# Kernel optimization log

Measured on AMD Instinct MI355X. Metric: run time of the kernel, lower is better.

The kernel has to match this reference:

```python
import jax, jax.numpy as jnp
import numpy as np

DMODEL = 1024
NHEAD = 16
DHEAD = DMODEL // NHEAD

def _layernorm(x, g, b, eps=1e-5):
    mu = jnp.mean(x, axis=-1, keepdims=True)
    var = jnp.var(x, axis=-1, keepdims=True)
    return (x - mu) * jax.lax.rsqrt(var + eps) * g + b

def setup_inputs() -> dict:
    key = jax.random.key(0)
    ks = jax.random.split(key, 12)
    b, lq, lv, d = 2, 2048, 2048, DMODEL
    s = 1.0 / np.sqrt(d)
    return {
        "q": jax.random.normal(ks[0], (b, lq, d), jnp.float32),
        "k": jax.random.normal(ks[1], (b, lv, d), jnp.float32),
        "v": jax.random.normal(ks[2], (b, lv, d), jnp.float32),
        "qln_g": jnp.ones((d,), jnp.float32),
        "qln_b": jnp.zeros((d,), jnp.float32),
        "kvln_g": jnp.ones((d,), jnp.float32),
        "kvln_b": jnp.zeros((d,), jnp.float32),
        "Wq": jax.random.normal(ks[3], (d, d), jnp.float32) * s,
        "Wk": jax.random.normal(ks[4], (d, d), jnp.float32) * s,
        "Wv": jax.random.normal(ks[5], (d, d), jnp.float32) * s,
        "Wg": jax.random.normal(ks[6], (d, d), jnp.float32) * s,
        "bg": jnp.zeros((d,), jnp.float32),
        "Wo": jax.random.normal(ks[7], (d, d), jnp.float32) * s,
    }

def reference(q, k, v, qln_g, qln_b, kvln_g, kvln_b, Wq, Wk, Wv, Wg, bg, Wo):
    b, lq, d = q.shape
    lv = v.shape[1]
    qn = _layernorm(q, qln_g, qln_b)           # [b, lq, d]
    q_ = qn @ Wq.T
    kk = _layernorm(k, kvln_g, kvln_b) @ Wk.T
    vv = _layernorm(v, kvln_g, kvln_b) @ Wv.T
    qh = q_.reshape(b, lq, NHEAD, DHEAD)       # bqhd
    kh = kk.reshape(b, lv, NHEAD, DHEAD)
    vh = vv.reshape(b, lv, NHEAD, DHEAD)
    scores = jnp.einsum('bqhd,bkhd->bhqk', qh, kh) / np.sqrt(DHEAD)
    attn = jax.nn.softmax(scores, axis=-1)
    y = jnp.einsum('bhqk,bkhd->bqhd', attn, vh).reshape(b, lq, d)
    g = jax.nn.sigmoid(qn @ Wg.T + bg)
    return (y * g) @ Wo.T
```

## Files before the change

kernel.cpp:

```cpp
#include <hip/hip_runtime.h>
#include <hip/hip_bf16.h>

#define DMODEL 1024
#define NHEAD  16
#define DHEAD  64
#define BATCH  2
#define LQ     2048
#define LV     2048
#define ROWS   (BATCH*LQ)
#define WELEMS (DMODEL*DMODEL)
#define BH     (BATCH*NHEAD)

typedef short bf16x8 __attribute__((ext_vector_type(8)));
typedef float f32x4  __attribute__((ext_vector_type(4)));

__device__ __forceinline__ float bf2f(unsigned short s) {
    union { unsigned u; float f; } v; v.u = ((unsigned)s) << 16;
    return v.f;
}
__device__ __forceinline__ unsigned pk_bf(float a, float b) {
    union { __hip_bfloat162 h; unsigned u; } c;
    c.h = __float22bfloat162_rn(make_float2(a, b));
    return c.u;
}

__device__ __forceinline__ void cp16_g2l(const void* g, void* l) {
    __builtin_amdgcn_global_load_lds(
        (const __attribute__((address_space(1))) void*)g,
        (__attribute__((address_space(3))) void*)l,
        16, 0, 0);
}

#define QSCALE (0.125f * 1.4426950408889634f)

__global__ __launch_bounds__(256) void prep_kernel(
    const float* q, const float* k, const float* v,
    const float* qg, const float* qb, const float* kvg, const float* kvb,
    const float* Wq, const float* Wk, const float* Wv, const float* Wg, const float* Wo,
    unsigned short* qn, unsigned short* kn, unsigned short* vn, unsigned short* wb)
{
    __shared__ float rs[4], rq[4];
    int z = blockIdx.y;
    if (z < 5) {
        if (blockIdx.x >= WELEMS / 1024) return;
        const float* srcs[5] = {Wq, Wk, Wv, Wg, Wo};
        const float* s = srcs[z];
        unsigned short* d = wb + (size_t)z * WELEMS;
        int i = (blockIdx.x * 256 + threadIdx.x) * 4;
        float4 x = *(const float4*)(s + i);
        uint2 o = make_uint2(pk_bf(x.x, x.y), pk_bf(x.z, x.w));
        *(uint2*)(d + i) = o;
        return;
    }
    int row = blockIdx.x;
    const float *x, *gp, *bp; unsigned short* o;
    if      (z == 5) { x = q; gp = qg;  bp = qb;  o = qn; }
    else if (z == 6) { x = k; gp = kvg; bp = kvb; o = kn; }
    else             { x = v; gp = kvg; bp = kvb; o = vn; }

    int col = threadIdx.x * 4;
    float4 xv = *(const float4*)(x + (size_t)row * DMODEL + col);
    float s  = xv.x + xv.y + xv.z + xv.w;
    float sq = xv.x*xv.x + xv.y*xv.y + xv.z*xv.z + xv.w*xv.w;
    #pragma unroll
    for (int off = 1; off < 64; off <<= 1) { s += __shfl_xor(s, off); sq += __shfl_xor(sq, off); }

    int wave = threadIdx.x >> 6, lane = threadIdx.x & 63;
    if (lane == 0) { rs[wave] = s; rq[wave] = sq; }
    __syncthreads();
    float ts = rs[0] + rs[1] + rs[2] + rs[3];
    float tq = rq[0] + rq[1] + rq[2] + rq[3];
    float mu  = ts * (1.0f / DMODEL);
    float var = tq * (1.0f / DMODEL) - mu * mu;
    float inv = rsqrtf(var + 1e-5f);

    float4 gv = *(const float4*)(gp + col);
    float4 bv = *(const float4*)(bp + col);
    float r0 = (xv.x - mu) * inv * gv.x + bv.x;
    float r1 = (xv.y - mu) * inv * gv.y + bv.y;
    float r2 = (xv.z - mu) * inv * gv.z + bv.z;
    float r3 = (xv.w - mu) * inv * gv.w + bv.w;
    *(uint2*)(o + (size_t)row * DMODEL + col) = make_uint2(pk_bf(r0, r1), pk_bf(r2, r3));
}

template<int MODE>
__device__ __forceinline__ void gemm256_core(
    const unsigned short* A, const unsigned short* Bw,
    unsigned short* Obf, const float* bias, float scale,
    unsigned short* Al, unsigned short* Bl, int bm, int bn)
{
    int tid  = threadIdx.x;
    int w = tid >> 6, l = tid & 63, quad = l >> 4, L = l & 15;
    int wm = w >> 2, wn = w & 3;

    int srow = w * 16 + (l >> 2);
    int scol = (l & 3) * 8;
    const unsigned short* gA = A  + (size_t)(bm * 256 + srow) * DMODEL + scol;
    const unsigned short* gB = Bw + (size_t)(bn * 256 + srow) * DMODEL + scol;
    int dstE = w * 512;

    #define STG_A(t) do { const unsigned short* s_ = gA + (t) * 32;           \
        unsigned short* d_ = Al + ((t) & 3) * 8192 + dstE;                    \
        cp16_g2l(s_, d_); cp16_g2l(s_ + 128 * DMODEL, d_ + 4096); } while (0)
    #define STG_B(t) do { const unsigned short* s_ = gB + (t) * 32;           \
        unsigned short* d_ = Bl + ((t) & 3) * 8192 + dstE;                    \
        cp16_g2l(s_, d_); cp16_g2l(s_ + 128 * DMODEL, d_ + 4096); } while (0)

    f32x4 acc[8][4];
    #pragma unroll
    for (int i = 0; i < 8; ++i)
        #pragma unroll
        for (int j = 0; j < 4; ++j) acc[i][j] = (f32x4){0.f, 0.f, 0.f, 0.f};

    STG_A(0); STG_B(0);
    STG_A(1); STG_B(1);
    STG_A(2); STG_B(2);
    asm volatile("s_waitcnt vmcnt(8)" ::: "memory");
    __builtin_amdgcn_s_barrier();

    const int NT = DMODEL / 32;
    for (int t = 0; t < NT; ++t) {
        const unsigned short* Ab = Al + (t & 3) * 8192 + wm * 4096;
        const unsigned short* Bb = Bl + (t & 3) * 8192 + wn * 2048;
        bf16x8 bfr[4], af[4];

        #pragma unroll
        for (int j = 0; j < 4; ++j)
            bfr[j] = *(const bf16x8*)&Bb[(j * 16 + L) * 32 + quad * 8];
        #pragma unroll
        for (int i2 = 0; i2 < 4; ++i2)
            af[i2] = *(const bf16x8*)&Ab[(i2 * 16 + L) * 32 + quad * 8];
        if (t + 3 < NT) STG_A(t + 3);
        __builtin_amdgcn_s_barrier();
        __builtin_amdgcn_s_setprio(1);
        #pragma unroll
        for (int i2 = 0; i2 < 4; ++i2)
            #pragma unroll
            for (int j = 0; j < 4; ++j) {
                if (MODE == 3)
                    acc[i2][j] = __builtin_amdgcn_mfma_f32_16x16x32_bf16(af[i2], bfr[j], acc[i2][j], 0, 0, 0);
                else
                    acc[i2][j] = __builtin_amdgcn_mfma_f32_16x16x32_bf16(bfr[j], af[i2], acc[i2][j], 0, 0, 0);
            }
        __builtin_amdgcn_s_setprio(0);
        __builtin_amdgcn_s_barrier();

        #pragma unroll
        for (int i2 = 0; i2 < 4; ++i2)
            af[i2] = *(const bf16x8*)&Ab[((64 + i2 * 16) + L) * 32 + quad * 8];
        if (t + 3 < NT) STG_B(t + 3);
        __builtin_amdgcn_s_barrier();
        __builtin_amdgcn_s_setprio(1);
        #pragma unroll
        for (int i2 = 0; i2 < 4; ++i2)
            #pragma unroll
            for (int j = 0; j < 4; ++j) {
                if (MODE == 3)
                    acc[4 + i2][j] = __builtin_amdgcn_mfma_f32_16x16x32_bf16(af[i2], bfr[j], acc[4 + i2][j], 0, 0, 0);
                else
                    acc[4 + i2][j] = __builtin_amdgcn_mfma_f32_16x16x32_bf16(bfr[j], af[i2], acc[4 + i2][j], 0, 0, 0);
            }
        __builtin_amdgcn_s_setprio(0);
        if      (t < NT - 3) asm volatile("s_waitcnt vmcnt(8)" ::: "memory");
        else if (t == NT - 3) asm volatile("s_waitcnt vmcnt(4)" ::: "memory");
        else if (t == NT - 2) asm volatile("s_waitcnt vmcnt(0)" ::: "memory");
        __builtin_amdgcn_s_barrier();
    }
    #undef STG_A
    #undef STG_B

    #pragma unroll
    for (int i = 0; i < 8; ++i) {
        #pragma unroll
        for (int j = 0; j < 4; ++j) {
            f32x4 a = acc[i][j];
            if (MODE == 3) {
                int gcol  = bn * 256 + wn * 64 + j * 16 + L;
                int grow0 = bm * 256 + wm * 128 + i * 16 + quad * 4;
                int b = grow0 >> 11, key0 = grow0 & 2047;
                int h = gcol >> 6,   dd   = gcol & 63;
                uint2 o = make_uint2(pk_bf(a[0], a[1]), pk_bf(a[2], a[3]));
                *(uint2*)&Obf[(((size_t)(b * NHEAD + h) * DHEAD + dd) << 11) + key0] = o;
            } else {
                int grow  = bm * 256 + wm * 128 + i * 16 + L;
                int gcol0 = bn * 256 + wn * 64 + j * 16 + quad * 4;
                size_t idx = (size_t)grow * DMODEL + gcol0;
                if (MODE == 0) {
                    uint2 o = make_uint2(pk_bf(a[0] * scale, a[1] * scale),
                                         pk_bf(a[2] * scale, a[3] * scale));
                    *(uint2*)&Obf[idx] = o;
                } else {
                    float4 bv = *(const float4*)&bias[gcol0];
                    float s0 = 1.0f / (1.0f + __expf(-(a[0] + bv.x)));
                    float s1 = 1.0f / (1.0f + __expf(-(a[1] + bv.y)));
                    float s2 = 1.0f / (1.0f + __expf(-(a[2] + bv.z)));
                    float s3 = 1.0f / (1.0f + __expf(-(a[3] + bv.w)));
                    *(uint2*)&Obf[idx] = make_uint2(pk_bf(s0, s1), pk_bf(s2, s3));
                }
            }
        }
    }
}

__global__ __launch_bounds__(512, 2) void gemm256_kernel(
    const unsigned short* qn, const unsigned short* kn, const unsigned short* vn,
    const unsigned short* wb,
    unsigned short* qs, unsigned short* kkp, unsigned short* vt, unsigned short* gate,
    const float* bg)
{
    __shared__ __align__(16) unsigned short Al[4 * 256 * 32];
    __shared__ __align__(16) unsigned short Bl[4 * 256 * 32];
    int f = blockIdx.x, xcd = f & 7, s = f >> 3;
    int z  = xcd & 3;
    int bm = ((xcd >> 2) << 3) | (s >> 2);
    int bn = s & 3;
    switch (z) {
        case 0:  gemm256_core<0>(qn, wb + 0 * WELEMS, qs,   nullptr, QSCALE, Al, Bl, bm, bn); break;
        case 1:  gemm256_core<0>(kn, wb + 1 * WELEMS, kkp,  nullptr, 1.0f,   Al, Bl, bm, bn); break;
        case 2:  gemm256_core<3>(vn, wb + 2 * WELEMS, vt,   nullptr, 1.0f,   Al, Bl, bm, bn); break;
        default: gemm256_core<1>(qn, wb + 3 * WELEMS, gate, bg,      1.0f,   Al, Bl, bm, bn); break;
    }
}

template<int MODE>
__device__ __forceinline__ void gemm_bt_core(
    const unsigned short* A, const unsigned short* Bw,
    unsigned short* Obf, float* Of32, const float* bias, float scale,
    unsigned short* Al, unsigned short* Bl, int bm, int bn)
{
    int tid  = threadIdx.x;
    int wave = tid >> 6, lane = tid & 63, quad = lane >> 4, L = lane & 15;
    int wm = wave >> 1, wn = wave & 1;

    int srow = wave * 16 + (lane >> 2);
    int scol = (lane & 3) * 8;
    const unsigned short* gA = A  + (size_t)(bm * 128 + srow) * DMODEL + scol;
    const unsigned short* gB = Bw + (size_t)(bn * 128 + srow) * DMODEL + scol;
    int lofs0 = wave * 16 * 32;
    int lofs1 = (64 + wave * 16) * 32;

    f32x4 acc[4][4];
    #pragma unroll
    for (int i = 0; i < 4; ++i)
        #pragma unroll
        for (int j = 0; j < 4; ++j) acc[i][j] = (f32x4){0.f, 0.f, 0.f, 0.f};

    cp16_g2l(gA,               Al + lofs0);
    cp16_g2l(gA + 64 * DMODEL, Al + lofs1);
    cp16_g2l(gB,               Bl + lofs0);
    cp16_g2l(gB + 64 * DMODEL, Bl + lofs1);

    int buf = 0;
    for (int k0 = 0; k0 < DMODEL; k0 += 32, buf ^= 1) {
        __syncthreads();
        if (k0 + 32 < DMODEL) {
            int nb = (buf ^ 1) * (128 * 32);
            cp16_g2l(gA + k0 + 32,               Al + nb + lofs0);
            cp16_g2l(gA + 64 * DMODEL + k0 + 32, Al + nb + lofs1);
            cp16_g2l(gB + k0 + 32,               Bl + nb + lofs0);
            cp16_g2l(gB + 64 * DMODEL + k0 + 32, Bl + nb + lofs1);
        }
        const unsigned short* Ab = Al + buf * (128 * 32);
        const unsigned short* Bb = Bl + buf * (128 * 32);
        bf16x8 af[4], bfr[4];
        #pragma unroll
        for (int i = 0; i < 4; ++i)
            af[i] = *(const bf16x8*)&Ab[(wm * 64 + i * 16 + L) * 32 + quad * 8];
        #pragma unroll
        for (int j = 0; j < 4; ++j)
            bfr[j] = *(const bf16x8*)&Bb[(wn * 64 + j * 16 + L) * 32 + quad * 8];
        #pragma unroll
        for (int i = 0; i < 4; ++i)
            #pragma unroll
            for (int j = 0; j < 4; ++j) {
                if (MODE == 3)
                    acc[i][j] = __builtin_amdgcn_mfma_f32_16x16x32_bf16(af[i], bfr[j], acc[i][j], 0, 0, 0);
                else
                    acc[i][j] = __builtin_amdgcn_mfma_f32_16x16x32_bf16(bfr[j], af[i], acc[i][j], 0, 0, 0);
            }
    }

    #pragma unroll
    for (int i = 0; i < 4; ++i) {
        #pragma unroll
        for (int j = 0; j < 4; ++j) {
            f32x4 a = acc[i][j];
            int grow  = bm * 128 + wm * 64 + i * 16 + L;
            int gcol0 = bn * 128 + wn * 64 + j * 16 + quad * 4;
            size_t idx = (size_t)grow * DMODEL + gcol0;
            if (MODE == 2) {
                *(f32x4*)&Of32[idx] = a;
            } else if (MODE == 0) {
                uint2 o = make_uint2(pk_bf(a[0] * scale, a[1] * scale),
                                     pk_bf(a[2] * scale, a[3] * scale));
                *(uint2*)&Obf[idx] = o;
            }
        }
    }
}

__device__ __forceinline__ void xcd_map(int& bm, int& bn) {
    int f = blockIdx.y * 8 + blockIdx.x;
    int xcd = f & 7, s = f >> 3;
    bn = s & 7;
    bm = ((s >> 3) << 3) | xcd;
}

__global__ __launch_bounds__(256) void gemm_f32out_kernel(
    const unsigned short* A, const unsigned short* Bw, float* O)
{
    __shared__ __align__(16) unsigned short Al[2 * 128 * 32];
    __shared__ __align__(16) unsigned short Bl[2 * 128 * 32];
    int bm, bn; xcd_map(bm, bn);
    gemm_bt_core<2>(A, Bw, nullptr, O, nullptr, 1.0f, Al, Bl, bm, bn);
}

__global__ __launch_bounds__(256, 4) void attn_kernel(
    const unsigned short* qs, const unsigned short* kk, const unsigned short* vt,
    const unsigned short* gate, unsigned short* yg)
{
    __shared__ __align__(16) unsigned short Kl[2 * 64 * 64];
    __shared__ __align__(16) unsigned short Vl[2 * 64 * 64];

    int tid  = threadIdx.x;
    int wave = tid >> 6, lane = tid & 63, quad = lane >> 4, L = lane & 15;

    int f  = blockIdx.y * 32 + blockIdx.x;
    int bh = (f & 7) * 4 + ((f >> 3) & 3);
    int qt = f >> 5;
    int bb = bh >> 4, h = bh & 15;
    int q0 = qt * 64;

    const unsigned short* Qb =
        qs + ((size_t)(bb * LQ + q0 + wave * 16 + L)) * DMODEL + h * DHEAD;
    bf16x8 aq0 = *(const bf16x8*)(Qb + quad * 8);
    bf16x8 aq1 = *(const bf16x8*)(Qb + 32 + quad * 8);

    f32x4 acc[4];
    #pragma unroll
    for (int nt = 0; nt < 4; ++nt) acc[nt] = (f32x4){0.f, 0.f, 0.f, 0.f};
    f32x4 lacc = (f32x4){0.f, 0.f, 0.f, 0.f};
    bf16x8 ones;
    #pragma unroll
    for (int j = 0; j < 8; ++j) ones[j] = (short)0x3F80;

    int rloc = lane >> 3;
    int c16  = (lane & 7) ^ rloc;
    int key0 = (wave & 1) * 32 + (rloc >> 2) * 8 + (wave >> 1) * 4 + (rloc & 3);

    const unsigned short* gK = kk + (size_t)bb * LV * DMODEL + h * DHEAD
                                  + (size_t)key0 * DMODEL + c16 * 8;
    const unsigned short* gV = vt + ((size_t)((bb * NHEAD + h) * DHEAD
                                  + wave * 16 + rloc)) * LV + c16 * 8;
    char* KlB = (char*)Kl;
    char* VlB = (char*)Vl;
    int dst0 = wave * 2048;

    cp16_g2l(gK,               KlB + dst0);
    cp16_g2l(gK + 16 * DMODEL, KlB + dst0 + 1024);
    cp16_g2l(gV,               VlB + dst0);
    cp16_g2l(gV + 8 * LV,      VlB + dst0 + 1024);

    int sl0 = (quad ^ (L & 7)) * 8;
    int buf = 0;
    for (int it = 0; it < LV / 64; ++it, buf ^= 1) {
        __syncthreads();
        if (it + 1 < LV / 64) {
            gK += 64 * DMODEL; gV += 64;
            int nb = (buf ^ 1) * 8192 + dst0;
            cp16_g2l(gK,               KlB + nb);
            cp16_g2l(gK + 16 * DMODEL, KlB + nb + 1024);
            cp16_g2l(gV,               VlB + nb);
            cp16_g2l(gV + 8 * LV,      VlB + nb + 1024);
        }
        const unsigned short* Kb = Kl + buf * 4096;
        const unsigned short* Vb = Vl + buf * 4096;

        f32x4 zz[4];
        __builtin_amdgcn_s_setprio(1);
        #pragma unroll
        for (int kt = 0; kt < 4; ++kt) {
            bf16x8 bk0 = *(const bf16x8*)&Kb[(kt * 16 + L) * 64 + sl0];
            bf16x8 bk1 = *(const bf16x8*)&Kb[(kt * 16 + L) * 64 + (sl0 ^ 32)];
            f32x4 z = (f32x4){0.f, 0.f, 0.f, 0.f};
            z = __builtin_amdgcn_mfma_f32_16x16x32_bf16(bk0, aq0, z, 0, 0, 0);
            z = __builtin_amdgcn_mfma_f32_16x16x32_bf16(bk1, aq1, z, 0, 0, 0);
            zz[kt] = z;
        }
        __builtin_amdgcn_s_setprio(0);

        union { unsigned u[4]; bf16x8 h; } pa0, pa1;
        pa0.u[0] = pk_bf(__builtin_amdgcn_exp2f(zz[0][0]), __builtin_amdgcn_exp2f(zz[0][1]));
        pa0.u[1] = pk_bf(__builtin_amdgcn_exp2f(zz[0][2]), __builtin_amdgcn_exp2f(zz[0][3]));
        pa0.u[2] = pk_bf(__builtin_amdgcn_exp2f(zz[2][0]), __builtin_amdgcn_exp2f(zz[2][1]));
        pa0.u[3] = pk_bf(__builtin_amdgcn_exp2f(zz[2][2]), __builtin_amdgcn_exp2f(zz[2][3]));
        pa1.u[0] = pk_bf(__builtin_amdgcn_exp2f(zz[1][0]), __builtin_amdgcn_exp2f(zz[1][1]));
        pa1.u[1] = pk_bf(__builtin_amdgcn_exp2f(zz[1][2]), __builtin_amdgcn_exp2f(zz[1][3]));
        pa1.u[2] = pk_bf(__builtin_amdgcn_exp2f(zz[3][0]), __builtin_amdgcn_exp2f(zz[3][1]));
        pa1.u[3] = pk_bf(__builtin_amdgcn_exp2f(zz[3][2]), __builtin_amdgcn_exp2f(zz[3][3]));

        __builtin_amdgcn_s_setprio(1);
        lacc = __builtin_amdgcn_mfma_f32_16x16x32_bf16(ones, pa0.h, lacc, 0, 0, 0);
        lacc = __builtin_amdgcn_mfma_f32_16x16x32_bf16(ones, pa1.h, lacc, 0, 0, 0);
        #pragma unroll
        for (int nt = 0; nt < 4; ++nt) {
            bf16x8 vb0 = *(const bf16x8*)&Vb[(nt * 16 + L) * 64 + sl0];
            bf16x8 vb1 = *(const bf16x8*)&Vb[(nt * 16 + L) * 64 + (sl0 ^ 32)];
            acc[nt] = __builtin_amdgcn_mfma_f32_16x16x32_bf16(vb0, pa0.h, acc[nt], 0, 0, 0);
            acc[nt] = __builtin_amdgcn_mfma_f32_16x16x32_bf16(vb1, pa1.h, acc[nt], 0, 0, 0);
        }
        __builtin_amdgcn_s_setprio(0);
    }

    float inv_l = 1.0f / lacc[0];
    size_t rb = ((size_t)(bb * LQ + q0 + wave * 16 + L)) * DMODEL + h * DHEAD;
    #pragma unroll
    for (int nt = 0; nt < 4; ++nt) {
        size_t idx = rb + nt * 16 + quad * 4;
        ushort4 g = *(const ushort4*)&gate[idx];
        float y0 = acc[nt][0] * inv_l * bf2f(g.x);
        float y1 = acc[nt][1] * inv_l * bf2f(g.y);
        float y2 = acc[nt][2] * inv_l * bf2f(g.z);
        float y3 = acc[nt][3] * inv_l * bf2f(g.w);
        *(uint2*)&yg[idx] = make_uint2(pk_bf(y0, y1), pk_bf(y2, y3));
    }
}

extern "C" void kernel_launch(void* const* d_in, const int* in_sizes, int n_in,
                              void* d_out, int out_size, void* d_ws, size_t ws_size,
                              hipStream_t stream)
{
    const float* q      = (const float*)d_in[0];
    const float* k      = (const float*)d_in[1];
    const float* v      = (const float*)d_in[2];
    const float* qln_g  = (const float*)d_in[3];
    const float* qln_b  = (const float*)d_in[4];
    const float* kvln_g = (const float*)d_in[5];
    const float* kvln_b = (const float*)d_in[6];
    const float* Wq     = (const float*)d_in[7];
    const float* Wk     = (const float*)d_in[8];
    const float* Wv     = (const float*)d_in[9];
    const float* Wg     = (const float*)d_in[10];
    const float* bg     = (const float*)d_in[11];
    const float* Wo     = (const float*)d_in[12];
    float* out = (float*)d_out;

    const size_t T8 = (size_t)ROWS * DMODEL * 2;
    char* ws = (char*)d_ws;
    unsigned short* qn   = (unsigned short*)(ws + 0 * T8);
    unsigned short* kn   = (unsigned short*)(ws + 1 * T8);
    unsigned short* vn   = (unsigned short*)(ws + 2 * T8);
    unsigned short* qs   = (unsigned short*)(ws + 3 * T8);
    unsigned short* kkp  = (unsigned short*)(ws + 4 * T8);
    unsigned short* vt   = (unsigned short*)(ws + 5 * T8);
    unsigned short* gate = (unsigned short*)(ws + 6 * T8);
    unsigned short* yg   = (unsigned short*)(ws + 7 * T8);
    unsigned short* wb   = (unsigned short*)(ws + 8 * T8);

    prep_kernel<<<dim3(ROWS, 8), 256, 0, stream>>>(
        q, k, v, qln_g, qln_b, kvln_g, kvln_b, Wq, Wk, Wv, Wg, Wo, qn, kn, vn, wb);
    gemm256_kernel<<<dim3(256), 512, 0, stream>>>(
        qn, kn, vn, wb, qs, kkp, vt, gate, bg);
    attn_kernel<<<dim3(32, 32), 256, 0, stream>>>(qs, kkp, vt, gate, yg);
    gemm_f32out_kernel<<<dim3(DMODEL / 128, ROWS / 128), 256, 0, stream>>>(yg, wb + 4 * WELEMS, out);
}
```

Before: 239.9 us.

## Restructure projection GEMM to BK=64 double-buffered tiles with XOR-swizzled LDS

The fused QKV/gate projection GEMM moves from a 4-stage ring of K=32 tiles with split A/B staging and four barriers per step to a 2-stage double buffer of K=64 tiles with one load-wait-barrier sequence per step. LDS rows are XOR-swizzled on both the global-to-LDS copy and the fragment reads to avoid bank conflicts. The aim is fewer barriers and waitcnt stalls per MFMA and cleaner LDS access. In exchange, prefetch depth drops from three tiles to one, so global latency may be harder to hide.

```diff
diff --git a/kernel.cpp b/kernel.cpp
--- a/kernel.cpp
+++ b/kernel.cpp
@@ -93,18 +93,27 @@
     int w = tid >> 6, l = tid & 63, quad = l >> 4, L = l & 15;
     int wm = w >> 2, wn = w & 3;
 
-    int srow = w * 16 + (l >> 2);
-    int scol = (l & 3) * 8;
-    const unsigned short* gA = A  + (size_t)(bm * 256 + srow) * DMODEL + scol;
-    const unsigned short* gB = Bw + (size_t)(bn * 256 + srow) * DMODEL + scol;
-    int dstE = w * 512;
-
-    #define STG_A(t) do { const unsigned short* s_ = gA + (t) * 32;           \
-        unsigned short* d_ = Al + ((t) & 3) * 8192 + dstE;                    \
-        cp16_g2l(s_, d_); cp16_g2l(s_ + 128 * DMODEL, d_ + 4096); } while (0)
-    #define STG_B(t) do { const unsigned short* s_ = gB + (t) * 32;           \
-        unsigned short* d_ = Bl + ((t) & 3) * 8192 + dstE;                    \
-        cp16_g2l(s_, d_); cp16_g2l(s_ + 128 * DMODEL, d_ + 4096); } while (0)
+    int c16 = (l & 7) ^ (l >> 3);
+    const unsigned short* gAs = A  + (size_t)(bm * 256 + w * 32 + (l >> 3)) * DMODEL + c16 * 8;
+    const unsigned short* gBs = Bw + (size_t)(bn * 256 + w * 32 + (l >> 3)) * DMODEL + c16 * 8;
+    int dstE = w * 2048;
+
+    #define STG_A(t) do { const unsigned short* s_ = gAs + (t) * 64;          \
+        unsigned short* d_ = Al + (((t) & 1) * 16384) + dstE;                 \
+        cp16_g2l(s_,              d_);                                        \
+        cp16_g2l(s_ +  8 * DMODEL, d_ +  512);                                \
+        cp16_g2l(s_ + 16 * DMODEL, d_ + 1024);                                \
+        cp16_g2l(s_ + 24 * DMODEL, d_ + 1536); } while (0)
+    #define STG_B(t) do { const unsigned short* s_ = gBs + (t) * 64;          \
+        unsigned short* d_ = Bl + (((t) & 1) * 16384) + dstE;                 \
+        cp16_g2l(s_,              d_);                                        \
+        cp16_g2l(s_ +  8 * DMODEL, d_ +  512);                                \
+        cp16_g2l(s_ + 16 * DMODEL, d_ + 1024);                                \
+        cp16_g2l(s_ + 24 * DMODEL, d_ + 1536); } while (0)
+
+    int sw = (L & 7) << 3;
+    int o0 = ( 0 + quad * 8) ^ sw;
+    int o1 = (32 + quad * 8) ^ sw;
 
     f32x4 acc[8][4];
     #pragma unroll
@@ -113,57 +122,40 @@
         for (int j = 0; j < 4; ++j) acc[i][j] = (f32x4){0.f, 0.f, 0.f, 0.f};
 
     STG_A(0); STG_B(0);
-    STG_A(1); STG_B(1);
-    STG_A(2); STG_B(2);
-    asm volatile("s_waitcnt vmcnt(8)" ::: "memory");
-    __builtin_amdgcn_s_barrier();
-
-    const int NT = DMODEL / 32;
-    for (int t = 0; t < NT; ++t) {
-        const unsigned short* Ab = Al + (t & 3) * 8192 + wm * 4096;
-        const unsigned short* Bb = Bl + (t & 3) * 8192 + wn * 2048;
-        bf16x8 bfr[4], af[4];
-
-        #pragma unroll
-        for (int j = 0; j < 4; ++j)
-            bfr[j] = *(const bf16x8*)&Bb[(j * 16 + L) * 32 + quad * 8];
-        #pragma unroll
-        for (int i2 = 0; i2 < 4; ++i2)
-            af[i2] = *(const bf16x8*)&Ab[(i2 * 16 + L) * 32 + quad * 8];
-        if (t + 3 < NT) STG_A(t + 3);
+
+    const int NT = DMODEL / 64;
+    for (int g = 0; g < NT; ++g) {
+        int s = g & 1;
+        if (g + 1 < NT) { STG_A(g + 1); STG_B(g + 1); }
+        if (g + 1 < NT) asm volatile("s_waitcnt vmcnt(8)" ::: "memory");
+        else            asm volatile("s_waitcnt vmcnt(0)" ::: "memory");
         __builtin_amdgcn_s_barrier();
+
+        const unsigned short* Ab = Al + s * 16384 + (wm * 128) * 64;
+        const unsigned short* Bb = Bl + s * 16384 + (wn * 64) * 64;
+        bf16x8 bfr[4][2];
+        #pragma unroll
+        for (int j = 0; j < 4; ++j) {
+            bfr[j][0] = *(const bf16x8*)&Bb[(j * 16 + L) * 64 + o0];
+            bfr[j][1] = *(const bf16x8*)&Bb[(j * 16 + L) * 64 + o1];
+        }
         __builtin_amdgcn_s_setprio(1);
         #pragma unroll
-        for (int i2 = 0; i2 < 4; ++i2)
+        for (int i2 = 0; i2 < 8; ++i2) {
+            bf16x8 a0 = *(const bf16x8*)&Ab[(i2 * 16 + L) * 64 + o0];
+            bf16x8 a1 = *(const bf16x8*)&Ab[(i2 * 16 + L) * 64 + o1];
             #pragma unroll
             for (int j = 0; j < 4; ++j) {
-                if (MODE == 3)
-                    acc[i2][j] = __builtin_amdgcn_mfma_f32_16x16x32_bf16(af[i2], bfr[j], acc[i2][j], 0, 0, 0);
-                else
-                    acc[i2][j] = __builtin_amdgcn_mfma_f32_16x16x32_bf16(bfr[j], af[i2], acc[i2][j], 0, 0, 0);
+                if (MODE == 3) {
+                    acc[i2][j] = __builtin_amdgcn_mfma_f32_16x16x32_bf16(a0, bfr[j][0], acc[i2][j], 0, 0, 0);
+                    acc[i2][j] = __builtin_amdgcn_mfma_f32_16x16x32_bf16(a1, bfr[j][1], acc[i2][j], 0, 0, 0);
+                } else {
+                    acc[i2][j] = __builtin_amdgcn_mfma_f32_16x16x32_bf16(bfr[j][0], a0, acc[i2][j], 0, 0, 0);
+                    acc[i2][j] = __builtin_amdgcn_mfma_f32_16x16x32_bf16(bfr[j][1], a1, acc[i2][j], 0, 0, 0);
+                }
             }
+        }
         __builtin_amdgcn_s_setprio(0);
-        __builtin_amdgcn_s_barrier();
-
-        #pragma unroll
-        for (int i2 = 0; i2 < 4; ++i2)
-            af[i2] = *(const bf16x8*)&Ab[((64 + i2 * 16) + L) * 32 + quad * 8];
-        if (t + 3 < NT) STG_B(t + 3);
-        __builtin_amdgcn_s_barrier();
-        __builtin_amdgcn_s_setprio(1);
-        #pragma unroll
-        for (int i2 = 0; i2 < 4; ++i2)
-            #pragma unroll
-            for (int j = 0; j < 4; ++j) {
-                if (MODE == 3)
-                    acc[4 + i2][j] = __builtin_amdgcn_mfma_f32_16x16x32_bf16(af[i2], bfr[j], acc[4 + i2][j], 0, 0, 0);
-                else
-                    acc[4 + i2][j] = __builtin_amdgcn_mfma_f32_16x16x32_bf16(bfr[j], af[i2], acc[4 + i2][j], 0, 0, 0);
-            }
-        __builtin_amdgcn_s_setprio(0);
-        if      (t < NT - 3) asm volatile("s_waitcnt vmcnt(8)" ::: "memory");
-        else if (t == NT - 3) asm volatile("s_waitcnt vmcnt(4)" ::: "memory");
-        else if (t == NT - 2) asm volatile("s_waitcnt vmcnt(0)" ::: "memory");
         __builtin_amdgcn_s_barrier();
     }
     #undef STG_A
@@ -208,8 +200,8 @@
     unsigned short* qs, unsigned short* kkp, unsigned short* vt, unsigned short* gate,
     const float* bg)
 {
-    __shared__ __align__(16) unsigned short Al[4 * 256 * 32];
-    __shared__ __align__(16) unsigned short Bl[4 * 256 * 32];
+    __shared__ __align__(16) unsigned short Al[2 * 256 * 64];
+    __shared__ __align__(16) unsigned short Bl[2 * 256 * 64];
     int f = blockIdx.x, xcd = f & 7, s = f >> 3;
     int z  = xcd & 3;
     int bm = ((xcd >> 2) << 3) | (s >> 2);
```

New measurement: 236.0 us. About the same (-1.6%).
